# Optimization experiments

Measured on AMD Instinct MI355X. Metric: run time of the kernel, lower is better.

Reference implementation:

```python
import jax, jax.numpy as jnp
import numpy as np

B, T, DIM = 1, 2048, 1024
NUM_HEADS, HEAD_DIM = 8, 128
ATTN_SCALE = 0.12


def _rms_norm(x):
    # F.rms_norm(x, x.size(-1)) with no weight; eps defaults to machine eps
    eps = jnp.asarray(jnp.finfo(x.dtype).eps, x.dtype)
    return x * jax.lax.rsqrt(jnp.mean(x * x, axis=-1, keepdims=True) + eps)


def _rotary_tables(seq_len, head_dim):
    # (1/1024) ** linspace(0,1,head_dim//4), then pad with head_dim//4 zeros
    freq = (1.0 / 1024.0) ** jnp.linspace(0.0, 1.0, head_dim // 4, dtype=jnp.float32)
    ang = jnp.concatenate([freq, jnp.zeros(head_dim // 4, jnp.float32)])  # [hd/2]
    theta = jnp.arange(seq_len, dtype=jnp.float32)[:, None] * ang[None, :]  # [T, hd/2]
    return jnp.cos(theta), jnp.sin(theta)


def _apply_rotary(x, cos, sin):
    # x: [B, T, H, hd]
    x1, x2 = jnp.split(x.astype(jnp.float32), 2, axis=-1)
    c = cos[None, :, None, :]
    s = sin[None, :, None, :]
    y1 = x1 * c + x2 * s
    y2 = -x1 * s + x2 * c
    return jnp.concatenate([y1, y2], axis=-1).astype(x.dtype)


def setup_inputs() -> dict:
    key = jax.random.key(0)
    ks = jax.random.split(key, 5)
    bound = (3.0 ** 0.5) * 0.5 * DIM ** (-0.5)
    x = jax.random.normal(ks[0], (B, T, DIM), jnp.float32)
    ve = jax.random.normal(ks[1], (B, T, NUM_HEADS * HEAD_DIM), jnp.float32)
    qkv_w = jax.random.uniform(ks[2], (3, NUM_HEADS * HEAD_DIM, DIM), jnp.float32, -bound, bound)
    lambdas = jnp.array([0.5, 0.5], jnp.float32)
    # original zero-inits c_proj; use small random weight so the output is nontrivial
    c_proj_w = jax.random.uniform(ks[3], (DIM, NUM_HEADS * HEAD_DIM), jnp.float32, -bound, bound)
    return {"x": x, "ve": ve, "qkv_w": qkv_w, "lambdas": lambdas, "c_proj_w": c_proj_w}


def reference(x, ve, qkv_w, lambdas, c_proj_w):
    Bx, Tx, D = x.shape
    H, hd = NUM_HEADS, HEAD_DIM
    # fused QKV projection: weight [3*H*hd, D]
    qkv = x @ qkv_w.reshape(3 * H * hd, D).T            # [B, T, 3*H*hd]
    qkv = qkv.reshape(Bx, Tx, 3 * H, hd)
    q, k, v = jnp.split(qkv, 3, axis=-2)                # each [B, T, H, hd]
    q, k = _rms_norm(q), _rms_norm(k)
    cos, sin = _rotary_tables(Tx, hd)
    q, k = _apply_rotary(q, cos, sin), _apply_rotary(k, cos, sin)
    v = lambdas[0] * v + lambdas[1] * ve.reshape(v.shape)
    att = jnp.einsum('bthd,bshd->bhts', q, k) * ATTN_SCALE
    causal = jnp.tril(jnp.ones((Tx, Tx), bool))
    att = jnp.where(causal[None, None], att, -jnp.inf)
    att = jax.nn.softmax(att, axis=-1)
    y = jnp.einsum('bhts,bshd->bthd', att, v).reshape(Bx, Tx, H * hd)
    return y @ c_proj_w.T
```

## Files before the change

kernel.cpp:

```cpp
#include <hip/hip_runtime.h>


typedef __attribute__((ext_vector_type(8))) short short8;
typedef __attribute__((ext_vector_type(4))) short short4b;
typedef __attribute__((ext_vector_type(4))) float fx4;
typedef __attribute__((ext_vector_type(8))) unsigned short ushort8;
typedef __attribute__((ext_vector_type(4))) unsigned short ushort4v;
typedef __attribute__((ext_vector_type(2))) unsigned short ushort2v;
typedef __attribute__((ext_vector_type(4))) float float4v;

#define T_SEQ 2048
#define NH 8
#define HD 128

__device__ __forceinline__ unsigned short f2bf(float f) {
  union { float f; unsigned u; } v; v.f = f;
  unsigned u = v.u;
  u += 0x7fffu + ((u >> 16) & 1u);
  return (unsigned short)(u >> 16);
}
__device__ __forceinline__ short bf_t(float f) {
  union { float f; unsigned u; } v; v.f = f;
  return (short)(v.u >> 16);
}
__device__ __forceinline__ float bf2f(unsigned short h) {
  union { unsigned u; float f; } v; v.u = ((unsigned)h) << 16;
  return v.f;
}

typedef __attribute__((address_space(1))) unsigned int glb_u32;
typedef __attribute__((address_space(3))) unsigned int lds_u32;
__device__ __forceinline__ void gl_lds16(const unsigned short* g, unsigned short* l) {
  __builtin_amdgcn_global_load_lds((const glb_u32*)g, (lds_u32*)l, 16, 0, 0);
}

__global__ __launch_bounds__(256) void cast3_kernel(
    const float* __restrict__ x, const float* __restrict__ w1,
    const float* __restrict__ w2, unsigned short* __restrict__ o) {
  long q = (long)blockIdx.x * 256 + threadIdx.x;
  const float* src;
  if (q < 524288)        src = x  + 4 * q;
  else if (q < 1310720)  src = w1 + 4 * (q - 524288);
  else                   src = w2 + 4 * (q - 1310720);
  float4v v = *(const float4v*)src;
  ushort4v r;
  r[0] = f2bf(v[0]); r[1] = f2bf(v[1]); r[2] = f2bf(v[2]); r[3] = f2bf(v[3]);
  *(ushort4v*)(o + 4 * q) = r;
}

template <bool OUT_BF16, int BM, int BN>
__global__ __launch_bounds__(256) void gemm_bt3(
    const unsigned short* __restrict__ A, const unsigned short* __restrict__ B,
    void* __restrict__ Cp, int M, int N, int K) {
  constexpr int MT = BM / 32;
  constexpr int NT = BN / 32;
  constexpr int ASEG = BM / 8;
  constexpr int NLOAD = (BM + BN) / 32;
  __shared__ unsigned short a_sh[BM * 64];
  __shared__ unsigned short b_sh[BN * 64];
  const int tid = threadIdx.x;
  const int wave = tid >> 6, lane = tid & 63;
  const int ln = lane & 15, quad = lane >> 4;
  const int wm = wave & 1, wn = wave >> 1;
  const long arow0 = (long)blockIdx.y * BM;
  const long brow0 = (long)blockIdx.x * BN;

  const unsigned short* gsrc[NLOAD];
  unsigned short* ldst[NLOAD];
  for (int i = 0; i < NLOAD; ++i) {
    int s = wave * NLOAD + i;
    int isB = s >= ASEG;
    int srel = isB ? s - ASEG : s;
    int li = srel * 64 + lane;
    int row = li >> 3, posc = li & 7;
    int c = posc ^ (row & 7);
    gsrc[i] = (isB ? B + brow0 * (long)K : A + arow0 * (long)K)
              + (long)row * K + c * 8;
    ldst[i] = (isB ? b_sh : a_sh) + srel * 512;
  }

  fx4 acc[MT][NT] = {};
  for (int k0 = 0; k0 < K; k0 += 64) {
    __syncthreads();
    for (int i = 0; i < NLOAD; ++i)
      gl_lds16(gsrc[i] + k0, ldst[i]);
    __syncthreads();
    short8 af[2][MT], bfr[2][NT];
    for (int kq = 0; kq < 2; ++kq) {
      for (int mt = 0; mt < MT; ++mt) {
        int m = wm * (BM / 2) + mt * 16 + ln;
        int pos = (kq * 4 + quad) ^ (m & 7);
        af[kq][mt] = *(const short8*)&a_sh[m * 64 + pos * 8];
      }
      for (int nt = 0; nt < NT; ++nt) {
        int n = wn * (BN / 2) + nt * 16 + ln;
        int pos = (kq * 4 + quad) ^ (n & 7);
        bfr[kq][nt] = *(const short8*)&b_sh[n * 64 + pos * 8];
      }
    }
    for (int kq = 0; kq < 2; ++kq)
      for (int mt = 0; mt < MT; ++mt)
        for (int nt = 0; nt < NT; ++nt)
          acc[mt][nt] = __builtin_amdgcn_mfma_f32_16x16x32_bf16(
              af[kq][mt], bfr[kq][nt], acc[mt][nt], 0, 0, 0);
  }
  for (int mt = 0; mt < MT; ++mt)
    for (int nt = 0; nt < NT; ++nt)
      for (int r = 0; r < 4; ++r) {
        long row = arow0 + wm * (BM / 2) + mt * 16 + quad * 4 + r;
        long col = brow0 + wn * (BN / 2) + nt * 16 + ln;
        float v = acc[mt][nt][r];
        if constexpr (OUT_BF16)
          ((unsigned short*)Cp)[row * N + col] = f2bf(v);
        else
          ((float*)Cp)[row * N + col] = v;
      }
}

__global__ __launch_bounds__(256) void qk_norm_rope(
    const unsigned short* __restrict__ qkv, unsigned short* __restrict__ qh,
    unsigned short* __restrict__ kh) {
  const int t = blockIdx.x;
  const int tid = threadIdx.x;
  const int h = tid >> 5, c = tid & 31;
  float cv[2], sv[2];
  for (int u = 0; u < 2; ++u) {
    int dd = 2 * c + u;
    if (dd < 32) {
      float ang = exp2f(-10.0f * (float)dd / 31.0f);
      float th = (float)t * ang;
      sv[u] = __sinf(th); cv[u] = __cosf(th);
    } else { sv[u] = 0.f; cv[u] = 1.f; }
  }
  for (int which = 0; which < 2; ++which) {
    const unsigned short* src = qkv + (long)t * 3072 + which * 1024 + h * 128;
    ushort2v aa = *(const ushort2v*)(src + 2 * c);
    ushort2v bb = *(const ushort2v*)(src + 64 + 2 * c);
    float x1[2] = { bf2f(aa[0]), bf2f(aa[1]) };
    float x2[2] = { bf2f(bb[0]), bf2f(bb[1]) };
    float ss = x1[0]*x1[0] + x1[1]*x1[1] + x2[0]*x2[0] + x2[1]*x2[1];
    for (int off = 1; off < 32; off <<= 1) ss += __shfl_xor(ss, off);
    float rn = rsqrtf(ss * (1.0f / 128.0f) + 1.1920929e-7f);
    ushort2v o1, o2;
    for (int u = 0; u < 2; ++u) {
      float y1 = ( x1[u] * cv[u] + x2[u] * sv[u]) * rn;
      float y2 = (-x1[u] * sv[u] + x2[u] * cv[u]) * rn;
      o1[u] = f2bf(y1); o2[u] = f2bf(y2);
    }
    unsigned short* dst = (which ? kh : qh) + ((long)h * T_SEQ + t) * 128;
    *(ushort2v*)(dst + 2 * c) = o1;
    *(ushort2v*)(dst + 64 + 2 * c) = o2;
  }
}

__global__ __launch_bounds__(256) void v_combine_t(
    const unsigned short* __restrict__ qkv, const float* __restrict__ ve,
    const float* __restrict__ lambdas, unsigned short* __restrict__ vt) {
  __shared__ unsigned short lt[128 * 72];
  const int tt = blockIdx.x, h = blockIdx.y;
  const int tid = threadIdx.x;
  const float l0 = lambdas[0], l1 = lambdas[1];
  const int r = tid >> 2, cb = (tid & 3) * 32;
  const unsigned short* vs = qkv + (long)(tt * 64 + r) * 3072 + 2048 + h * 128 + cb;
  const float* es = ve + (long)(tt * 64 + r) * 1024 + h * 128 + cb;
  ushort8 vv[4];
  for (int q = 0; q < 4; ++q) vv[q] = *(const ushort8*)(vs + 8 * q);
  float4v ee[8];
  for (int q = 0; q < 8; ++q) ee[q] = *(const float4v*)(es + 4 * q);
  for (int j = 0; j < 32; ++j) {
    float v = bf2f(vv[j >> 3][j & 7]) * l0 + ee[j >> 2][j & 3] * l1;
    lt[(cb + j) * 72 + r] = f2bf(v);
  }
  __syncthreads();
  const int d = tid >> 1, half = tid & 1;
  unsigned short* dst = vt + ((long)h * HD + d) * T_SEQ + tt * 64 + half * 32;
  const unsigned short* srcl = &lt[d * 72];
  for (int g = 0; g < 8; ++g) {
    int p0 = half * 32 + g * 4;
    int kv0 = ((p0 >> 5) & 1) * 32 + ((p0 >> 2) & 1) * 16 + ((p0 >> 3) & 3) * 4;
    *(ushort4v*)(dst + g * 4) = *(const ushort4v*)(srcl + kv0);
  }
}

#define ATT_C1 0.17312340490667562f
#define ATT_C2 23.083120654223415f

__global__ __launch_bounds__(256, 3) void attn_part(
    const unsigned short* __restrict__ qh, const unsigned short* __restrict__ kh,
    const unsigned short* __restrict__ vt, unsigned short* __restrict__ Yp,
    float* __restrict__ lp) {
  __shared__ unsigned short kbuf[8192];
  __shared__ unsigned short vbuf[2][8192];
  const int tid = threadIdx.x;
  const int wave = tid >> 6, lane = tid & 63;
  const int ln = lane & 15, quad = lane >> 4;
  const int qt = blockIdx.x, h = blockIdx.y, ch = blockIdx.z;
  const int jmax = 2 * qt + 1;
  const int j0 = ch * 4;
  if (j0 > jmax) return;
  const int j1 = min(j0 + 3, jmax);

  int qg[2];
  short8 qf[2][4];
  for (int s = 0; s < 2; ++s) {
    qg[s] = qt * 128 + wave * 32 + s * 16 + ln;
    const unsigned short* qbase = qh + ((long)h * T_SEQ + qg[s]) * 128;
    for (int kc = 0; kc < 4; ++kc)
      qf[s][kc] = *(const short8*)(qbase + kc * 32 + quad * 8);
  }
  fx4 accy[2][8] = {};
  float l_loc[2] = {0.f, 0.f};

  const unsigned short* kg[4]; unsigned short* kl[4];
  const unsigned short* vg[4]; unsigned short* vl[4];
  for (int i = 0; i < 4; ++i) {
    int s = wave * 4 + i;
    { int li = s * 64 + lane; int row = li >> 4, posc = li & 15;
      int c = posc ^ (row & 15);
      kg[i] = kh + ((long)h * T_SEQ + row) * 128 + c * 8;
      kl[i] = &kbuf[s * 512]; }
    { int li = s * 64 + lane; int row = li >> 3, posc = li & 7;
      int c = posc ^ (row & 7);
      vg[i] = vt + ((long)h * HD + row) * T_SEQ + c * 8;
      vl[i] = &vbuf[0][s * 512]; }
  }
  for (int i = 0; i < 4; ++i) gl_lds16(kg[i] + (long)j0 * 8192, kl[i]);
  for (int i = 0; i < 4; ++i) gl_lds16(vg[i] + (long)j0 * 64, vl[i]);

  int cur = 0;
  for (int jt = j0; jt <= j1; ++jt, cur ^= 1) {
    __syncthreads();
    fx4 s4[2][4];
    for (int kt = 0; kt < 4; ++kt) {
      s4[0][kt] = fx4{0.f, 0.f, 0.f, 0.f};
      s4[1][kt] = fx4{0.f, 0.f, 0.f, 0.f};
      for (int kc = 0; kc < 4; ++kc) {
        int pos = (kc * 4 + quad) ^ ln;
        short8 kf = *(const short8*)&kbuf[(kt * 16 + ln) * 128 + pos * 8];
        s4[0][kt] = __builtin_amdgcn_mfma_f32_16x16x32_bf16(kf, qf[0][kc], s4[0][kt], 0, 0, 0);
        s4[1][kt] = __builtin_amdgcn_mfma_f32_16x16x32_bf16(kf, qf[1][kc], s4[1][kt], 0, 0, 0);
      }
    }
    __syncthreads();
    if (jt < j1) {
      for (int i = 0; i < 4; ++i) gl_lds16(kg[i] + (long)(jt + 1) * 8192, kl[i]);
      for (int i = 0; i < 4; ++i) gl_lds16(vg[i] + (long)(jt + 1) * 64, vl[i] + (cur ^ 1) * 8192);
    }
    short4b pb[2][4];
    for (int s = 0; s < 2; ++s)
      for (int kt = 0; kt < 4; ++kt) {
        int kvb = jt * 64 + kt * 16 + quad * 4;
        float p[4];
        for (int r = 0; r < 4; ++r) {
          float pv = exp2f(fmaf(s4[s][kt][r], ATT_C1, -ATT_C2));
          p[r] = pv;
        }
        if (jt * 64 + kt * 16 + 15 > qt * 128 + wave * 32 + s * 16) {
          for (int r = 0; r < 4; ++r) if (kvb + r > qg[s]) p[r] = 0.f;
        }
        l_loc[s] += (p[0] + p[1]) + (p[2] + p[3]);
        pb[s][kt] = short4b{ bf_t(p[0]), bf_t(p[1]), bf_t(p[2]), bf_t(p[3]) };
      }
    const unsigned short* vb_ = &vbuf[cur][0];
    for (int kh2 = 0; kh2 < 2; ++kh2) {
      for (int dt = 0; dt < 8; ++dt) {
        int row = dt * 16 + ln;
        int pos = (kh2 * 4 + quad) ^ (ln & 7);
        short8 va = *(const short8*)&vb_[row * 64 + pos * 8];
        short4b va0 = { va[0], va[1], va[2], va[3] };
        short4b va1 = { va[4], va[5], va[6], va[7] };
        for (int s = 0; s < 2; ++s) {
          accy[s][dt] = __builtin_amdgcn_mfma_f32_16x16x16bf16_1k(
              va0, pb[s][kh2 * 2], accy[s][dt], 0, 0, 0);
          accy[s][dt] = __builtin_amdgcn_mfma_f32_16x16x16bf16_1k(
              va1, pb[s][kh2 * 2 + 1], accy[s][dt], 0, 0, 0);
        }
      }
    }
  }

  int cbase = qt + ((qt - 1) * (qt - 1)) / 4;
  const long pp = (long)(h * 72 + cbase + ch);
  for (int s = 0; s < 2; ++s) {
    float l = l_loc[s];
    l += __shfl_xor(l, 16);
    l += __shfl_xor(l, 32);
    int q = wave * 32 + s * 16 + ln;
    if (quad == 0) lp[pp * 128 + q] = l;
    unsigned short* yb = Yp + pp * 16384 + (long)q * 128;
    for (int dt = 0; dt < 8; ++dt) {
      ushort4v o;
      for (int r = 0; r < 4; ++r) o[r] = f2bf(accy[s][dt][r]);
      *(ushort4v*)(yb + dt * 16 + quad * 4) = o;
    }
  }
}

__global__ __launch_bounds__(256) void attn_combine(
    const unsigned short* __restrict__ Yp, const float* __restrict__ lp,
    unsigned short* __restrict__ y) {
  const int bx = blockIdx.x, h = blockIdx.y;
  const int qt = bx >> 1, sub = bx & 1;
  const int tid = threadIdx.x;
  const int row = sub * 64 + (tid >> 2), cb = (tid & 3) * 32;
  const int nc = (qt >> 1) + 1;
  const int cbase = qt + ((qt - 1) * (qt - 1)) / 4;
  float acc[32];
  for (int j = 0; j < 32; ++j) acc[j] = 0.f;
  float ltot = 0.f;
  for (int c = 0; c < nc; ++c) {
    long pp = (long)(h * 72 + cbase + c);
    const unsigned short* ys = Yp + pp * 16384 + (long)row * 128 + cb;
    ltot += lp[pp * 128 + row];
    for (int q8 = 0; q8 < 4; ++q8) {
      ushort8 v = *(const ushort8*)(ys + q8 * 8);
      for (int j = 0; j < 8; ++j) acc[q8 * 8 + j] += bf2f(v[j]);
    }
  }
  float inv = 1.f / ltot;
  unsigned short* dst = y + (long)(qt * 128 + row) * 1024 + h * 128 + cb;
  for (int q8 = 0; q8 < 4; ++q8) {
    ushort8 o;
    for (int j = 0; j < 8; ++j) o[j] = f2bf(acc[q8 * 8 + j] * inv);
    *(ushort8*)(dst + q8 * 8) = o;
  }
}

extern "C" void kernel_launch(void* const* d_in, const int* in_sizes, int n_in,
                              void* d_out, int out_size, void* d_ws, size_t ws_size,
                              hipStream_t stream) {
  const float* x       = (const float*)d_in[0];
  const float* ve      = (const float*)d_in[1];
  const float* qkv_w   = (const float*)d_in[2];
  const float* lambdas = (const float*)d_in[3];
  const float* c_proj  = (const float*)d_in[4];
  char* ws = (char*)d_ws;
  unsigned short* qkv_bf = (unsigned short*)(ws);
  unsigned short* x_bf   = (unsigned short*)(ws + 12582912);
  unsigned short* wqkv   = (unsigned short*)(ws + 16777216);
  unsigned short* wproj  = (unsigned short*)(ws + 23068672);
  unsigned short* qhat   = (unsigned short*)(ws + 25165824);
  unsigned short* khat   = (unsigned short*)(ws + 29360128);
  unsigned short* vtb    = (unsigned short*)(ws + 33554432);
  unsigned short* ybf    = (unsigned short*)(ws + 37748736);
  unsigned short* Yp     = (unsigned short*)(ws);
  float*          lpart  = (float*)(ws + 18874368);
  float* out = (float*)d_out;

  cast3_kernel<<<6144, 256, 0, stream>>>(x, qkv_w, c_proj, x_bf);
  gemm_bt3<true, 64, 128><<<dim3(24, 32), 256, 0, stream>>>(x_bf, wqkv, qkv_bf, 2048, 3072, 1024);
  qk_norm_rope<<<2048, 256, 0, stream>>>(qkv_bf, qhat, khat);
  v_combine_t<<<dim3(32, 8), 256, 0, stream>>>(qkv_bf, ve, lambdas, vtb);
  attn_part<<<dim3(16, 8, 8), 256, 0, stream>>>(qhat, khat, vtb, Yp, lpart);
  attn_combine<<<dim3(32, 8), 256, 0, stream>>>(Yp, lpart, ybf);
  gemm_bt3<false, 64, 64><<<dim3(16, 32), 256, 0, stream>>>(ybf, wproj, out, 2048, 1024, 1024);
}
```

Measured before the change: 206.9 us.

## Double-buffer GEMM and attention K tiles, fuse QK-norm/RoPE with V combine

The GEMM now keeps two LDS buffers for the A and B tiles. It prefetches the next K-slice while computing on the current one, which drops one barrier per iteration. The attention kernel also double-buffers K next to V, so the next K/V tile is issued right after the loop-top barrier, and its occupancy hint drops from 3 to 2 blocks per CU to fit the larger LDS footprint. The separate QK RMS-norm/RoPE and V-combine/transpose kernels are merged into one launch, saving a dispatch at the cost of fewer, heavier blocks for the norm work.

Measured after the change: 194.6 us. 1.06x faster.

```diff
diff --git a/kernel.cpp b/kernel.cpp
--- a/kernel.cpp
+++ b/kernel.cpp
@@ -49,15 +49,15 @@
 }
 
 template <bool OUT_BF16, int BM, int BN>
-__global__ __launch_bounds__(256) void gemm_bt3(
+__global__ __launch_bounds__(256) void gemm_bt4(
     const unsigned short* __restrict__ A, const unsigned short* __restrict__ B,
     void* __restrict__ Cp, int M, int N, int K) {
   constexpr int MT = BM / 32;
   constexpr int NT = BN / 32;
   constexpr int ASEG = BM / 8;
   constexpr int NLOAD = (BM + BN) / 32;
-  __shared__ unsigned short a_sh[BM * 64];
-  __shared__ unsigned short b_sh[BN * 64];
+  __shared__ unsigned short a_sh[2][BM * 64];
+  __shared__ unsigned short b_sh[2][BN * 64];
   const int tid = threadIdx.x;
   const int wave = tid >> 6, lane = tid & 63;
   const int ln = lane & 15, quad = lane >> 4;
@@ -67,6 +67,7 @@
 
   const unsigned short* gsrc[NLOAD];
   unsigned short* ldst[NLOAD];
+  int bstr[NLOAD];
   for (int i = 0; i < NLOAD; ++i) {
     int s = wave * NLOAD + i;
     int isB = s >= ASEG;
@@ -76,26 +77,31 @@
     int c = posc ^ (row & 7);
     gsrc[i] = (isB ? B + brow0 * (long)K : A + arow0 * (long)K)
               + (long)row * K + c * 8;
-    ldst[i] = (isB ? b_sh : a_sh) + srel * 512;
-  }
+    ldst[i] = (isB ? &b_sh[0][0] : &a_sh[0][0]) + srel * 512;
+    bstr[i] = isB ? BN * 64 : BM * 64;
+  }
+  for (int i = 0; i < NLOAD; ++i) gl_lds16(gsrc[i], ldst[i]);
 
   fx4 acc[MT][NT] = {};
-  for (int k0 = 0; k0 < K; k0 += 64) {
+  int cur = 0;
+  for (int k0 = 0; k0 < K; k0 += 64, cur ^= 1) {
     __syncthreads();
-    for (int i = 0; i < NLOAD; ++i)
-      gl_lds16(gsrc[i] + k0, ldst[i]);
-    __syncthreads();
+    if (k0 + 64 < K)
+      for (int i = 0; i < NLOAD; ++i)
+        gl_lds16(gsrc[i] + k0 + 64, ldst[i] + (cur ^ 1) * bstr[i]);
+    const unsigned short* ash = &a_sh[cur][0];
+    const unsigned short* bsh = &b_sh[cur][0];
     short8 af[2][MT], bfr[2][NT];
     for (int kq = 0; kq < 2; ++kq) {
       for (int mt = 0; mt < MT; ++mt) {
         int m = wm * (BM / 2) + mt * 16 + ln;
         int pos = (kq * 4 + quad) ^ (m & 7);
-        af[kq][mt] = *(const short8*)&a_sh[m * 64 + pos * 8];
+        af[kq][mt] = *(const short8*)&ash[m * 64 + pos * 8];
       }
       for (int nt = 0; nt < NT; ++nt) {
         int n = wn * (BN / 2) + nt * 16 + ln;
         int pos = (kq * 4 + quad) ^ (n & 7);
-        bfr[kq][nt] = *(const short8*)&b_sh[n * 64 + pos * 8];
+        bfr[kq][nt] = *(const short8*)&bsh[n * 64 + pos * 8];
       }
     }
     for (int kq = 0; kq < 2; ++kq)
@@ -117,79 +123,83 @@
       }
 }
 
-__global__ __launch_bounds__(256) void qk_norm_rope(
-    const unsigned short* __restrict__ qkv, unsigned short* __restrict__ qh,
-    unsigned short* __restrict__ kh) {
-  const int t = blockIdx.x;
-  const int tid = threadIdx.x;
-  const int h = tid >> 5, c = tid & 31;
-  float cv[2], sv[2];
-  for (int u = 0; u < 2; ++u) {
-    int dd = 2 * c + u;
-    if (dd < 32) {
-      float ang = exp2f(-10.0f * (float)dd / 31.0f);
-      float th = (float)t * ang;
-      sv[u] = __sinf(th); cv[u] = __cosf(th);
-    } else { sv[u] = 0.f; cv[u] = 1.f; }
-  }
-  for (int which = 0; which < 2; ++which) {
-    const unsigned short* src = qkv + (long)t * 3072 + which * 1024 + h * 128;
-    ushort2v aa = *(const ushort2v*)(src + 2 * c);
-    ushort2v bb = *(const ushort2v*)(src + 64 + 2 * c);
-    float x1[2] = { bf2f(aa[0]), bf2f(aa[1]) };
-    float x2[2] = { bf2f(bb[0]), bf2f(bb[1]) };
-    float ss = x1[0]*x1[0] + x1[1]*x1[1] + x2[0]*x2[0] + x2[1]*x2[1];
-    for (int off = 1; off < 32; off <<= 1) ss += __shfl_xor(ss, off);
-    float rn = rsqrtf(ss * (1.0f / 128.0f) + 1.1920929e-7f);
-    ushort2v o1, o2;
-    for (int u = 0; u < 2; ++u) {
-      float y1 = ( x1[u] * cv[u] + x2[u] * sv[u]) * rn;
-      float y2 = (-x1[u] * sv[u] + x2[u] * cv[u]) * rn;
-      o1[u] = f2bf(y1); o2[u] = f2bf(y2);
-    }
-    unsigned short* dst = (which ? kh : qh) + ((long)h * T_SEQ + t) * 128;
-    *(ushort2v*)(dst + 2 * c) = o1;
-    *(ushort2v*)(dst + 64 + 2 * c) = o2;
-  }
-}
-
-__global__ __launch_bounds__(256) void v_combine_t(
+__global__ __launch_bounds__(256) void prep_qkv(
     const unsigned short* __restrict__ qkv, const float* __restrict__ ve,
-    const float* __restrict__ lambdas, unsigned short* __restrict__ vt) {
+    const float* __restrict__ lambdas, unsigned short* __restrict__ qh,
+    unsigned short* __restrict__ kh, unsigned short* __restrict__ vt) {
   __shared__ unsigned short lt[128 * 72];
   const int tt = blockIdx.x, h = blockIdx.y;
   const int tid = threadIdx.x;
-  const float l0 = lambdas[0], l1 = lambdas[1];
-  const int r = tid >> 2, cb = (tid & 3) * 32;
-  const unsigned short* vs = qkv + (long)(tt * 64 + r) * 3072 + 2048 + h * 128 + cb;
-  const float* es = ve + (long)(tt * 64 + r) * 1024 + h * 128 + cb;
-  ushort8 vv[4];
-  for (int q = 0; q < 4; ++q) vv[q] = *(const ushort8*)(vs + 8 * q);
-  float4v ee[8];
-  for (int q = 0; q < 8; ++q) ee[q] = *(const float4v*)(es + 4 * q);
-  for (int j = 0; j < 32; ++j) {
-    float v = bf2f(vv[j >> 3][j & 7]) * l0 + ee[j >> 2][j & 3] * l1;
-    lt[(cb + j) * 72 + r] = f2bf(v);
-  }
-  __syncthreads();
-  const int d = tid >> 1, half = tid & 1;
-  unsigned short* dst = vt + ((long)h * HD + d) * T_SEQ + tt * 64 + half * 32;
-  const unsigned short* srcl = &lt[d * 72];
-  for (int g = 0; g < 8; ++g) {
-    int p0 = half * 32 + g * 4;
-    int kv0 = ((p0 >> 5) & 1) * 32 + ((p0 >> 2) & 1) * 16 + ((p0 >> 3) & 3) * 4;
-    *(ushort4v*)(dst + g * 4) = *(const ushort4v*)(srcl + kv0);
+
+  {
+    const int r2 = tid >> 5, c = tid & 31;
+    float ang[2];
+    for (int u = 0; u < 2; ++u) {
+      int dd = 2 * c + u;
+      ang[u] = (dd < 32) ? exp2f(-10.0f * (float)dd / 31.0f) : 0.0f;
+    }
+    for (int rr = 0; rr < 8; ++rr) {
+      int t = tt * 64 + rr * 8 + r2;
+      float cv[2], sv[2];
+      for (int u = 0; u < 2; ++u) {
+        float th = (float)t * ang[u];
+        sv[u] = __sinf(th); cv[u] = __cosf(th);
+      }
+      for (int which = 0; which < 2; ++which) {
+        const unsigned short* src = qkv + (long)t * 3072 + which * 1024 + h * 128;
+        ushort2v aa = *(const ushort2v*)(src + 2 * c);
+        ushort2v bb = *(const ushort2v*)(src + 64 + 2 * c);
+        float x1[2] = { bf2f(aa[0]), bf2f(aa[1]) };
+        float x2[2] = { bf2f(bb[0]), bf2f(bb[1]) };
+        float ss = x1[0]*x1[0] + x1[1]*x1[1] + x2[0]*x2[0] + x2[1]*x2[1];
+        for (int off = 1; off < 32; off <<= 1) ss += __shfl_xor(ss, off);
+        float rn = rsqrtf(ss * (1.0f / 128.0f) + 1.1920929e-7f);
+        ushort2v o1, o2;
+        for (int u = 0; u < 2; ++u) {
+          float y1 = ( x1[u] * cv[u] + x2[u] * sv[u]) * rn;
+          float y2 = (-x1[u] * sv[u] + x2[u] * cv[u]) * rn;
+          o1[u] = f2bf(y1); o2[u] = f2bf(y2);
+        }
+        unsigned short* dst = (which ? kh : qh) + ((long)h * T_SEQ + t) * 128;
+        *(ushort2v*)(dst + 2 * c) = o1;
+        *(ushort2v*)(dst + 64 + 2 * c) = o2;
+      }
+    }
+  }
+
+  {
+    const float l0 = lambdas[0], l1 = lambdas[1];
+    const int r = tid >> 2, cb = (tid & 3) * 32;
+    const unsigned short* vs = qkv + (long)(tt * 64 + r) * 3072 + 2048 + h * 128 + cb;
+    const float* es = ve + (long)(tt * 64 + r) * 1024 + h * 128 + cb;
+    ushort8 vv[4];
+    for (int q = 0; q < 4; ++q) vv[q] = *(const ushort8*)(vs + 8 * q);
+    float4v ee[8];
+    for (int q = 0; q < 8; ++q) ee[q] = *(const float4v*)(es + 4 * q);
+    for (int j = 0; j < 32; ++j) {
+      float v = bf2f(vv[j >> 3][j & 7]) * l0 + ee[j >> 2][j & 3] * l1;
+      lt[(cb + j) * 72 + r] = f2bf(v);
+    }
+    __syncthreads();
+    const int d = tid >> 1, half = tid & 1;
+    unsigned short* dst = vt + ((long)h * HD + d) * T_SEQ + tt * 64 + half * 32;
+    const unsigned short* srcl = &lt[d * 72];
+    for (int g = 0; g < 8; ++g) {
+      int p0 = half * 32 + g * 4;
+      int kv0 = ((p0 >> 5) & 1) * 32 + ((p0 >> 2) & 1) * 16 + ((p0 >> 3) & 3) * 4;
+      *(ushort4v*)(dst + g * 4) = *(const ushort4v*)(srcl + kv0);
+    }
   }
 }
 
 #define ATT_C1 0.17312340490667562f
 #define ATT_C2 23.083120654223415f
 
-__global__ __launch_bounds__(256, 3) void attn_part(
+__global__ __launch_bounds__(256, 2) void attn_part(
     const unsigned short* __restrict__ qh, const unsigned short* __restrict__ kh,
     const unsigned short* __restrict__ vt, unsigned short* __restrict__ Yp,
     float* __restrict__ lp) {
-  __shared__ unsigned short kbuf[8192];
+  __shared__ unsigned short kbuf[2][8192];
   __shared__ unsigned short vbuf[2][8192];
   const int tid = threadIdx.x;
   const int wave = tid >> 6, lane = tid & 63;
@@ -218,7 +228,7 @@
     { int li = s * 64 + lane; int row = li >> 4, posc = li & 15;
       int c = posc ^ (row & 15);
       kg[i] = kh + ((long)h * T_SEQ + row) * 128 + c * 8;
-      kl[i] = &kbuf[s * 512]; }
+      kl[i] = &kbuf[0][s * 512]; }
     { int li = s * 64 + lane; int row = li >> 3, posc = li & 7;
       int c = posc ^ (row & 7);
       vg[i] = vt + ((long)h * HD + row) * T_SEQ + c * 8;
@@ -230,31 +240,30 @@
   int cur = 0;
   for (int jt = j0; jt <= j1; ++jt, cur ^= 1) {
     __syncthreads();
+    if (jt < j1) {
+      int nb = (cur ^ 1) * 8192;
+      for (int i = 0; i < 4; ++i) gl_lds16(kg[i] + (long)(jt + 1) * 8192, kl[i] + nb);
+      for (int i = 0; i < 4; ++i) gl_lds16(vg[i] + (long)(jt + 1) * 64, vl[i] + nb);
+    }
+    const unsigned short* kb_ = &kbuf[cur][0];
     fx4 s4[2][4];
     for (int kt = 0; kt < 4; ++kt) {
       s4[0][kt] = fx4{0.f, 0.f, 0.f, 0.f};
       s4[1][kt] = fx4{0.f, 0.f, 0.f, 0.f};
       for (int kc = 0; kc < 4; ++kc) {
         int pos = (kc * 4 + quad) ^ ln;
-        short8 kf = *(const short8*)&kbuf[(kt * 16 + ln) * 128 + pos * 8];
+        short8 kf = *(const short8*)&kb_[(kt * 16 + ln) * 128 + pos * 8];
         s4[0][kt] = __builtin_amdgcn_mfma_f32_16x16x32_bf16(kf, qf[0][kc], s4[0][kt], 0, 0, 0);
         s4[1][kt] = __builtin_amdgcn_mfma_f32_16x16x32_bf16(kf, qf[1][kc], s4[1][kt], 0, 0, 0);
       }
-    }
-    __syncthreads();
-    if (jt < j1) {
-      for (int i = 0; i < 4; ++i) gl_lds16(kg[i] + (long)(jt + 1) * 8192, kl[i]);
-      for (int i = 0; i < 4; ++i) gl_lds16(vg[i] + (long)(jt + 1) * 64, vl[i] + (cur ^ 1) * 8192);
     }
     short4b pb[2][4];
     for (int s = 0; s < 2; ++s)
       for (int kt = 0; kt < 4; ++kt) {
         int kvb = jt * 64 + kt * 16 + quad * 4;
         float p[4];
-        for (int r = 0; r < 4; ++r) {
-          float pv = exp2f(fmaf(s4[s][kt][r], ATT_C1, -ATT_C2));
-          p[r] = pv;
-        }
+        for (int r = 0; r < 4; ++r)
+          p[r] = exp2f(fmaf(s4[s][kt][r], ATT_C1, -ATT_C2));
         if (jt * 64 + kt * 16 + 15 > qt * 128 + wave * 32 + s * 16) {
           for (int r = 0; r < 4; ++r) if (kvb + r > qg[s]) p[r] = 0.f;
         }
@@ -348,10 +357,9 @@
   float* out = (float*)d_out;
 
   cast3_kernel<<<6144, 256, 0, stream>>>(x, qkv_w, c_proj, x_bf);
-  gemm_bt3<true, 64, 128><<<dim3(24, 32), 256, 0, stream>>>(x_bf, wqkv, qkv_bf, 2048, 3072, 1024);
-  qk_norm_rope<<<2048, 256, 0, stream>>>(qkv_bf, qhat, khat);
-  v_combine_t<<<dim3(32, 8), 256, 0, stream>>>(qkv_bf, ve, lambdas, vtb);
+  gemm_bt4<true, 64, 128><<<dim3(24, 32), 256, 0, stream>>>(x_bf, wqkv, qkv_bf, 2048, 3072, 1024);
+  prep_qkv<<<dim3(32, 8), 256, 0, stream>>>(qkv_bf, ve, lambdas, qhat, khat, vtb);
   attn_part<<<dim3(16, 8, 8), 256, 0, stream>>>(qhat, khat, vtb, Yp, lpart);
   attn_combine<<<dim3(32, 8), 256, 0, stream>>>(Yp, lpart, ybf);
-  gemm_bt3<false, 64, 64><<<dim3(16, 32), 256, 0, stream>>>(ybf, wproj, out, 2048, 1024, 1024);
-}
+  gemm_bt4<false, 64, 64><<<dim3(16, 32), 256, 0, stream>>>(ybf, wproj, out, 2048, 1024, 1024);
+}
```
